# Performance work log

Measured on AMD Instinct MI355X. Metric: run time of the kernel, lower is better.

The kernel has to match this reference:

```python
import jax, jax.numpy as jnp
import numpy as np

E4M3 = jnp.float8_e4m3fn  # forward fp8 dtype (HYBRID recipe fwd)

def fp8_qdq(x, fp8_dtype):
    # quantize (scale=1) to fp8 then dequantize back: models precision loss
    return x.astype(fp8_dtype).astype(x.dtype)

def setup_inputs() -> dict:
    key = jax.random.key(0)
    k1, k2 = jax.random.split(key)
    tokens, d_in, units = 4096, 1024, 4096
    x = jax.random.normal(k1, (tokens, d_in), dtype=jnp.float32)
    # kernel_initializer default: RandomNormal(mean=0.0, stddev=0.023)
    kernel = jax.random.normal(k2, (d_in, units), dtype=jnp.float32) * 0.023
    bias = jnp.zeros((units,), dtype=jnp.float32)
    return {"x": x, "kernel": kernel, "bias": bias}

def reference(x, kernel, bias):
    # fp8 quantize/dequantize prologue on activations and weights
    xq = fp8_qdq(x, E4M3)          # [tokens, d_in]
    kq = fp8_qdq(kernel, E4M3)     # [d_in, units]
    out = jnp.matmul(xq, kq) + bias  # [tokens, units]
    # gelu approximate=True (tanh approximation)
    return jax.nn.gelu(out, approximate=True)
```

## Files before the change

kernel.cpp:

```cpp
#include <hip/hip_runtime.h>
#include <hip/hip_bf16.h>

typedef float f32x4 __attribute__((ext_vector_type(4)));
typedef long  l2    __attribute__((ext_vector_type(2)));

__device__ __forceinline__ void gld16(const void* g, void* l) {
    __builtin_amdgcn_global_load_lds(
        (const __attribute__((address_space(1))) void*)g,
        (__attribute__((address_space(3))) void*)l,
        16, 0, 0);
}

__device__ __forceinline__ float gelu_tanh(float x) {
    float u = 0.7978845608028654f * x * (1.0f + 0.044715f * x * x);
    float e = __expf(2.0f * u);
    float t = 1.0f - 2.0f / (e + 1.0f);
    return 0.5f * x * (1.0f + t);
}


__global__ __launch_bounds__(256) void quant_fused_kernel(
        const float* __restrict__ x,  unsigned char* __restrict__ Aq,
        const float* __restrict__ w,  unsigned char* __restrict__ BTq,
        int nA, int K, int N) {
    __shared__ unsigned char lds[64 * 68];
    const int tid = threadIdx.x;

    if (blockIdx.x < nA) {
        int i = blockIdx.x * 256 + tid;
        float4 v = reinterpret_cast<const float4*>(x)[i];
        int pk = 0;
        pk = __builtin_amdgcn_cvt_pk_fp8_f32(v.x, v.y, pk, false);
        pk = __builtin_amdgcn_cvt_pk_fp8_f32(v.z, v.w, pk, true);
        const long k4 = (long)i * 4;
        const int  row = (int)(k4 / K);
        const int  k   = (int)(k4 % K);
        const int  o   = k & 63;
        const int  g   = (o & 31) >> 3;
        const int  s   = (o & 7) + ((o >> 5) & 1) * 8;
        const int  c   = g ^ ((row >> 1) & 3);
        *reinterpret_cast<unsigned int*>(
            Aq + (long)row * K + (k & ~63) + (c << 4) + s) = (unsigned int)pk;
        return;
    }

    const int bid = blockIdx.x - nA;
    const int n0 = (bid & (N / 64 - 1)) * 64;
    const int k0 = (bid / (N / 64)) * 64;

    #pragma unroll
    for (int p = 0; p < 4; ++p) {
        int s = p * 256 + tid;
        int r = s >> 4;
        int c = s & 15;
        float4 v = *reinterpret_cast<const float4*>(
            w + (long)(k0 + r) * N + n0 + c * 4);
        int pk = 0;
        pk = __builtin_amdgcn_cvt_pk_fp8_f32(v.x, v.y, pk, false);
        pk = __builtin_amdgcn_cvt_pk_fp8_f32(v.z, v.w, pk, true);
        *reinterpret_cast<unsigned int*>(&lds[r * 68 + c * 4]) = (unsigned int)pk;
    }
    __syncthreads();
    #pragma unroll
    for (int p = 0; p < 4; ++p) {
        int sidx = p * 256 + tid;
        int n  = sidx >> 4;
        int kg = sidx & 15;
        unsigned int wv = 0;
        #pragma unroll
        for (int j = 0; j < 4; ++j)
            wv |= (unsigned int)lds[(kg * 4 + j) * 68 + n] << (8 * j);
        const int nn = n0 + n;
        const int o  = kg * 4;
        const int g  = (o & 31) >> 3;
        const int s  = (o & 7) + ((o >> 5) & 1) * 8;
        const int c  = g ^ ((nn >> 1) & 3);
        *reinterpret_cast<unsigned int*>(
            BTq + (long)nn * K + k0 + (c << 4) + s) = wv;
    }
}

__global__ __launch_bounds__(512, 4) void gemm_fp8_kernel(
        const unsigned char* __restrict__ A,
        const unsigned char* __restrict__ BT,
        const float* __restrict__ bias,
        float* __restrict__ out,
        int M, int N, int K) {
    constexpr int BM = 128, BN = 256, BK = 64;
    __shared__ unsigned char lds[2][(BM + BN) * BK];

    const int tid  = threadIdx.x;
    const int lane = tid & 63;
    const int wid  = tid >> 6;
    const int wm   = wid >> 2;
    const int wn   = wid & 3;

    const int bid = blockIdx.x;
    const int xcd = bid & 7, idx = bid >> 3;
    const int tile_m = (xcd >> 1) * 8 + (idx & 7);
    const int tile_n = (xcd & 1) * 8 + (idx >> 3);
    const int m0 = tile_m * BM, n0 = tile_n * BN;

    const int lrow = lane & 15;
    const int kgrp = lane >> 4;
    const int chunkoff = ((kgrp ^ ((lrow >> 1) & 3)) << 4);

    const int srow   = tid >> 2;
    const int schunk = (tid & 3) << 4;
    const unsigned char* gA = A  + (long)(m0 + srow) * K + schunk;
    const unsigned char* gB = BT + (long)(n0 + srow) * K + schunk;

    const int aBase = (wm * 64 + lrow) * 64 + chunkoff;
    const int bBase = 8192 + (wn * 64 + lrow) * 64 + chunkoff;

    f32x4 acc[4][4] = {};

    const int NT = K / BK;

#define STAGE_A(BB, TT)                                                   \
    gld16(gA + (long)(TT) * BK, &lds[BB][wid * 1024])
#define STAGE_B(BB, H, TT)                                                \
    gld16(gB + (long)(H) * 128 * K + (long)(TT) * BK,                     \
          &lds[BB][8192 + (H) * 8192 + wid * 1024])

#define MFMA_Q(AI0, BJ0, AR, BR)                                          \
    _Pragma("unroll") for (int ks = 0; ks < 2; ++ks)                      \
    _Pragma("unroll") for (int fi = 0; fi < 2; ++fi)                      \
    _Pragma("unroll") for (int fj = 0; fj < 2; ++fj)                      \
        acc[(AI0) + fi][(BJ0) + fj] =                                     \
            __builtin_amdgcn_mfma_f32_16x16x32_fp8_fp8(                   \
                AR[fi][ks], BR[fj][ks], acc[(AI0) + fi][(BJ0) + fj], 0, 0, 0)

    STAGE_A(0, 0); STAGE_B(0, 0, 0); STAGE_B(0, 1, 0);
    asm volatile("s_waitcnt vmcnt(0)" ::: "memory");
    __builtin_amdgcn_s_barrier();

    for (int t = 0; t < NT; ++t) {
        const int cur = t & 1, nxt = cur ^ 1;
        const unsigned char* sL = &lds[cur][0];
        const bool st = (t + 1 < NT);
        l2 a01[2], a23[2], b01[2], b23[2];

        if (st) { STAGE_A(nxt, t + 1); STAGE_B(nxt, 0, t + 1); }
        #pragma unroll
        for (int f = 0; f < 2; ++f) {
            a01[f] = *reinterpret_cast<const l2*>(sL + aBase + f * 1024);
            b01[f] = *reinterpret_cast<const l2*>(sL + bBase + f * 1024);
            b23[f] = *reinterpret_cast<const l2*>(sL + bBase + 2048 + f * 1024);
        }
        __builtin_amdgcn_s_barrier();
        asm volatile("s_waitcnt lgkmcnt(0)" ::: "memory");
        __builtin_amdgcn_sched_barrier(0);
        __builtin_amdgcn_s_setprio(1);
        MFMA_Q(0, 0, a01, b01);
        MFMA_Q(0, 2, a01, b23);
        __builtin_amdgcn_s_setprio(0);

        if (st) { STAGE_B(nxt, 1, t + 1); }
        #pragma unroll
        for (int f = 0; f < 2; ++f)
            a23[f] = *reinterpret_cast<const l2*>(sL + aBase + 2048 + f * 1024);
        __builtin_amdgcn_s_barrier();
        asm volatile("s_waitcnt lgkmcnt(0)" ::: "memory");
        __builtin_amdgcn_sched_barrier(0);
        __builtin_amdgcn_s_setprio(1);
        MFMA_Q(2, 0, a23, b01);
        MFMA_Q(2, 2, a23, b23);
        __builtin_amdgcn_s_setprio(0);
        __builtin_amdgcn_sched_barrier(0);

        if (t < NT - 1) {
            asm volatile("s_waitcnt vmcnt(0)" ::: "memory");
            __builtin_amdgcn_sched_barrier(0);
            __builtin_amdgcn_s_barrier();
        }
    }

    __syncthreads();
    float* eplds = reinterpret_cast<float*>(&lds[0][0]) + wid * 1088;
    const int  col0   = n0 + wn * 64;
    const long rbase0 = m0 + wm * 64;
    float bv[4];
    #pragma unroll
    for (int bj = 0; bj < 4; ++bj) bv[bj] = bias[col0 + bj * 16 + lrow];

    #pragma unroll
    for (int ai = 0; ai < 4; ++ai) {
        #pragma unroll
        for (int bj = 0; bj < 4; ++bj) {
            #pragma unroll
            for (int r = 0; r < 4; ++r) {
                float xv = acc[ai][bj][r] + bv[bj];
                eplds[(kgrp * 4 + r) * 68 + bj * 16 + lrow] = gelu_tanh(xv);
            }
        }
        #pragma unroll
        for (int s = 0; s < 4; ++s) {
            f32x4 v = *reinterpret_cast<const f32x4*>(
                eplds + (s * 4 + kgrp) * 68 + lrow * 4);
            __builtin_nontemporal_store(v, reinterpret_cast<f32x4*>(
                out + (rbase0 + ai * 16 + s * 4 + kgrp) * N + col0 + lrow * 4));
        }
    }
#undef STAGE_A
#undef STAGE_B
#undef MFMA_Q
}

extern "C" void kernel_launch(void* const* d_in, const int* in_sizes, int n_in,
                              void* d_out, int out_size, void* d_ws, size_t ws_size,
                              hipStream_t stream) {
    const float* x    = (const float*)d_in[0];
    const float* w    = (const float*)d_in[1];
    const float* bias = (const float*)d_in[2];
    float* out = (float*)d_out;

    const int units  = in_sizes[2];
    const int dmodel = in_sizes[1] / units;
    const int tokens = in_sizes[0] / dmodel;

    unsigned char* Aq  = (unsigned char*)d_ws;
    unsigned char* BTq = Aq + (size_t)tokens * dmodel;

    const int nA = tokens * dmodel / 4 / 256;
    const int nB = (units / 64) * (dmodel / 64);
    quant_fused_kernel<<<dim3(nA + nB), dim3(256), 0, stream>>>(
        x, Aq, w, BTq, nA, dmodel, units);

    const int nblocks = (tokens / 128) * (units / 256);
    gemm_fp8_kernel<<<dim3(nblocks), dim3(512), 0, stream>>>(
        Aq, BTq, bias, out, tokens, units, dmodel);
}
```

Before: 47.36 us.

## Load GEMM operands directly from global into registers, drop LDS staging

Replaces the LDS double-buffered global_load_lds pipeline with direct per-lane global loads of pre-swizzled fp8 fragments into registers, software-pipelined two K-steps deep. The tile shrinks to 128x128 with 256-thread blocks, giving twice as many blocks, and the LDS is used only for the epilogue. This removes LDS traffic and barriers, but it gives up cross-wave reuse of each tile through LDS. Operands are re-fetched from L2 by each wave, and the loads are 16-byte strided reads spread across rows.

```diff
diff --git a/kernel.cpp b/kernel.cpp
--- a/kernel.cpp
+++ b/kernel.cpp
@@ -3,13 +3,6 @@
 
 typedef float f32x4 __attribute__((ext_vector_type(4)));
 typedef long  l2    __attribute__((ext_vector_type(2)));
-
-__device__ __forceinline__ void gld16(const void* g, void* l) {
-    __builtin_amdgcn_global_load_lds(
-        (const __attribute__((address_space(1))) void*)g,
-        (__attribute__((address_space(3))) void*)l,
-        16, 0, 0);
-}
 
 __device__ __forceinline__ float gelu_tanh(float x) {
     float u = 0.7978845608028654f * x * (1.0f + 0.044715f * x * x);
@@ -80,104 +73,65 @@
     }
 }
 
-__global__ __launch_bounds__(512, 4) void gemm_fp8_kernel(
+__global__ __launch_bounds__(256, 3) void gemm_fp8_kernel(
         const unsigned char* __restrict__ A,
         const unsigned char* __restrict__ BT,
         const float* __restrict__ bias,
         float* __restrict__ out,
         int M, int N, int K) {
-    constexpr int BM = 128, BN = 256, BK = 64;
-    __shared__ unsigned char lds[2][(BM + BN) * BK];
+    constexpr int BM = 128, BN = 128, BK = 64;
+    __shared__ float eplds_all[4][1088];
 
     const int tid  = threadIdx.x;
     const int lane = tid & 63;
     const int wid  = tid >> 6;
-    const int wm   = wid >> 2;
-    const int wn   = wid & 3;
+    const int wm   = wid >> 1, wn = wid & 1;
 
     const int bid = blockIdx.x;
     const int xcd = bid & 7, idx = bid >> 3;
-    const int tile_m = (xcd >> 1) * 8 + (idx & 7);
-    const int tile_n = (xcd & 1) * 8 + (idx >> 3);
+    const int tile_m = (xcd >> 1) * 8  + (idx & 7);
+    const int tile_n = (xcd & 1) * 16 + (idx >> 3);
     const int m0 = tile_m * BM, n0 = tile_n * BN;
 
     const int lrow = lane & 15;
     const int kgrp = lane >> 4;
     const int chunkoff = ((kgrp ^ ((lrow >> 1) & 3)) << 4);
 
-    const int srow   = tid >> 2;
-    const int schunk = (tid & 3) << 4;
-    const unsigned char* gA = A  + (long)(m0 + srow) * K + schunk;
-    const unsigned char* gB = BT + (long)(n0 + srow) * K + schunk;
-
-    const int aBase = (wm * 64 + lrow) * 64 + chunkoff;
-    const int bBase = 8192 + (wn * 64 + lrow) * 64 + chunkoff;
+    const unsigned char* pA[4];
+    const unsigned char* pB[4];
+    #pragma unroll
+    for (int f = 0; f < 4; ++f) {
+        pA[f] = A  + (long)(m0 + wm * 64 + f * 16 + lrow) * K + chunkoff;
+        pB[f] = BT + (long)(n0 + wn * 64 + f * 16 + lrow) * K + chunkoff;
+    }
 
     f32x4 acc[4][4] = {};
+    l2 aX[4], bX[4], aY[4], bY[4];
 
     const int NT = K / BK;
 
-#define STAGE_A(BB, TT)                                                   \
-    gld16(gA + (long)(TT) * BK, &lds[BB][wid * 1024])
-#define STAGE_B(BB, H, TT)                                                \
-    gld16(gB + (long)(H) * 128 * K + (long)(TT) * BK,                     \
-          &lds[BB][8192 + (H) * 8192 + wid * 1024])
-
-#define MFMA_Q(AI0, BJ0, AR, BR)                                          \
-    _Pragma("unroll") for (int ks = 0; ks < 2; ++ks)                      \
-    _Pragma("unroll") for (int fi = 0; fi < 2; ++fi)                      \
-    _Pragma("unroll") for (int fj = 0; fj < 2; ++fj)                      \
-        acc[(AI0) + fi][(BJ0) + fj] =                                     \
-            __builtin_amdgcn_mfma_f32_16x16x32_fp8_fp8(                   \
-                AR[fi][ks], BR[fj][ks], acc[(AI0) + fi][(BJ0) + fj], 0, 0, 0)
-
-    STAGE_A(0, 0); STAGE_B(0, 0, 0); STAGE_B(0, 1, 0);
-    asm volatile("s_waitcnt vmcnt(0)" ::: "memory");
-    __builtin_amdgcn_s_barrier();
-
-    for (int t = 0; t < NT; ++t) {
-        const int cur = t & 1, nxt = cur ^ 1;
-        const unsigned char* sL = &lds[cur][0];
-        const bool st = (t + 1 < NT);
-        l2 a01[2], a23[2], b01[2], b23[2];
-
-        if (st) { STAGE_A(nxt, t + 1); STAGE_B(nxt, 0, t + 1); }
-        #pragma unroll
-        for (int f = 0; f < 2; ++f) {
-            a01[f] = *reinterpret_cast<const l2*>(sL + aBase + f * 1024);
-            b01[f] = *reinterpret_cast<const l2*>(sL + bBase + f * 1024);
-            b23[f] = *reinterpret_cast<const l2*>(sL + bBase + 2048 + f * 1024);
-        }
-        __builtin_amdgcn_s_barrier();
-        asm volatile("s_waitcnt lgkmcnt(0)" ::: "memory");
-        __builtin_amdgcn_sched_barrier(0);
-        __builtin_amdgcn_s_setprio(1);
-        MFMA_Q(0, 0, a01, b01);
-        MFMA_Q(0, 2, a01, b23);
-        __builtin_amdgcn_s_setprio(0);
-
-        if (st) { STAGE_B(nxt, 1, t + 1); }
-        #pragma unroll
-        for (int f = 0; f < 2; ++f)
-            a23[f] = *reinterpret_cast<const l2*>(sL + aBase + 2048 + f * 1024);
-        __builtin_amdgcn_s_barrier();
-        asm volatile("s_waitcnt lgkmcnt(0)" ::: "memory");
-        __builtin_amdgcn_sched_barrier(0);
-        __builtin_amdgcn_s_setprio(1);
-        MFMA_Q(2, 0, a23, b01);
-        MFMA_Q(2, 2, a23, b23);
-        __builtin_amdgcn_s_setprio(0);
-        __builtin_amdgcn_sched_barrier(0);
-
-        if (t < NT - 1) {
-            asm volatile("s_waitcnt vmcnt(0)" ::: "memory");
-            __builtin_amdgcn_sched_barrier(0);
-            __builtin_amdgcn_s_barrier();
-        }
+#define LOADS(AS, BS, T)                                                  \
+    _Pragma("unroll") for (int f = 0; f < 4; ++f) {                       \
+        AS[f] = *reinterpret_cast<const l2*>(pA[f] + (T) * 64);           \
+        BS[f] = *reinterpret_cast<const l2*>(pB[f] + (T) * 64);           \
     }
 
-    __syncthreads();
-    float* eplds = reinterpret_cast<float*>(&lds[0][0]) + wid * 1088;
+#define MFMA_ALL(AR, BR)                                                  \
+    _Pragma("unroll") for (int ks = 0; ks < 2; ++ks)                      \
+    _Pragma("unroll") for (int fi = 0; fi < 4; ++fi)                      \
+    _Pragma("unroll") for (int fj = 0; fj < 4; ++fj)                      \
+        acc[fi][fj] = __builtin_amdgcn_mfma_f32_16x16x32_fp8_fp8(         \
+            AR[fi][ks], BR[fj][ks], acc[fi][fj], 0, 0, 0)
+
+    LOADS(aX, bX, 0);
+    for (int t = 0; t < NT; t += 2) {
+        LOADS(aY, bY, t + 1);
+        MFMA_ALL(aX, bX);
+        if (t + 2 < NT) { LOADS(aX, bX, t + 2); }
+        MFMA_ALL(aY, bY);
+    }
+
+    float* eplds = eplds_all[wid];
     const int  col0   = n0 + wn * 64;
     const long rbase0 = m0 + wm * 64;
     float bv[4];
@@ -202,9 +156,8 @@
                 out + (rbase0 + ai * 16 + s * 4 + kgrp) * N + col0 + lrow * 4));
         }
     }
-#undef STAGE_A
-#undef STAGE_B
-#undef MFMA_Q
+#undef LOADS
+#undef MFMA_ALL
 }
 
 extern "C" void kernel_launch(void* const* d_in, const int* in_sizes, int n_in,
@@ -227,7 +180,7 @@
     quant_fused_kernel<<<dim3(nA + nB), dim3(256), 0, stream>>>(
         x, Aq, w, BTq, nA, dmodel, units);
 
-    const int nblocks = (tokens / 128) * (units / 256);
-    gemm_fp8_kernel<<<dim3(nblocks), dim3(512), 0, stream>>>(
+    const int nblocks = (tokens / 128) * (units / 128);
+    gemm_fp8_kernel<<<dim3(nblocks), dim3(256), 0, stream>>>(
         Aq, BTq, bias, out, tokens, units, dmodel);
 }
```

After: 56.87 us. 20.1% more time.

## Shrink GEMM tile to 128x128 with 4x2 wave layout and higher occupancy

Applied to the files above, without the earlier changes.

Halves the GEMM block tile along N (BN 256 to 128) and remaps the 8 waves into a 4x2 grid, each holding a 32x64 accumulator instead of 64x64. The block count doubles and launch bounds are raised to 8 waves per SIMD, aiming for more resident blocks and less register pressure to better hide latency. Shared memory becomes a union so the epilogue scratch fits inside the smaller staging buffer. The cost is lower arithmetic intensity per block, with more global and LDS traffic per MFMA, and fewer MFMAs between barriers.

```diff
diff --git a/kernel.cpp b/kernel.cpp
--- a/kernel.cpp
+++ b/kernel.cpp
@@ -80,25 +80,28 @@
     }
 }
 
-__global__ __launch_bounds__(512, 4) void gemm_fp8_kernel(
+__global__ __launch_bounds__(512, 8) void gemm_fp8_kernel(
         const unsigned char* __restrict__ A,
         const unsigned char* __restrict__ BT,
         const float* __restrict__ bias,
         float* __restrict__ out,
         int M, int N, int K) {
-    constexpr int BM = 128, BN = 256, BK = 64;
-    __shared__ unsigned char lds[2][(BM + BN) * BK];
+    constexpr int BM = 128, BN = 128, BK = 64;
+    __shared__ union {
+        unsigned char buf[2][(BM + BN) * BK];
+        float ep[8][1088];
+    } sm;
 
     const int tid  = threadIdx.x;
     const int lane = tid & 63;
     const int wid  = tid >> 6;
-    const int wm   = wid >> 2;
-    const int wn   = wid & 3;
+    const int wm   = wid >> 1;
+    const int wn   = wid & 1;
 
     const int bid = blockIdx.x;
     const int xcd = bid & 7, idx = bid >> 3;
-    const int tile_m = (xcd >> 1) * 8 + (idx & 7);
-    const int tile_n = (xcd & 1) * 8 + (idx >> 3);
+    const int tile_m = (xcd >> 1) * 8  + (idx & 7);
+    const int tile_n = (xcd & 1) * 16 + (idx >> 3);
     const int m0 = tile_m * BM, n0 = tile_n * BN;
 
     const int lrow = lane & 15;
@@ -110,62 +113,57 @@
     const unsigned char* gA = A  + (long)(m0 + srow) * K + schunk;
     const unsigned char* gB = BT + (long)(n0 + srow) * K + schunk;
 
-    const int aBase = (wm * 64 + lrow) * 64 + chunkoff;
+    const int aBase = (wm * 32 + lrow) * 64 + chunkoff;
     const int bBase = 8192 + (wn * 64 + lrow) * 64 + chunkoff;
 
-    f32x4 acc[4][4] = {};
+    f32x4 acc[2][4] = {};
 
     const int NT = K / BK;
 
 #define STAGE_A(BB, TT)                                                   \
-    gld16(gA + (long)(TT) * BK, &lds[BB][wid * 1024])
-#define STAGE_B(BB, H, TT)                                                \
-    gld16(gB + (long)(H) * 128 * K + (long)(TT) * BK,                     \
-          &lds[BB][8192 + (H) * 8192 + wid * 1024])
-
-#define MFMA_Q(AI0, BJ0, AR, BR)                                          \
+    gld16(gA + (long)(TT) * BK, &sm.buf[BB][wid * 1024])
+#define STAGE_B(BB, TT)                                                   \
+    gld16(gB + (long)(TT) * BK, &sm.buf[BB][8192 + wid * 1024])
+
+#define MFMA_Q(BJ0, BR)                                                   \
     _Pragma("unroll") for (int ks = 0; ks < 2; ++ks)                      \
     _Pragma("unroll") for (int fi = 0; fi < 2; ++fi)                      \
     _Pragma("unroll") for (int fj = 0; fj < 2; ++fj)                      \
-        acc[(AI0) + fi][(BJ0) + fj] =                                     \
-            __builtin_amdgcn_mfma_f32_16x16x32_fp8_fp8(                   \
-                AR[fi][ks], BR[fj][ks], acc[(AI0) + fi][(BJ0) + fj], 0, 0, 0)
-
-    STAGE_A(0, 0); STAGE_B(0, 0, 0); STAGE_B(0, 1, 0);
+        acc[fi][(BJ0) + fj] = __builtin_amdgcn_mfma_f32_16x16x32_fp8_fp8( \
+            a01[fi][ks], BR[fj][ks], acc[fi][(BJ0) + fj], 0, 0, 0)
+
+    STAGE_A(0, 0); STAGE_B(0, 0);
     asm volatile("s_waitcnt vmcnt(0)" ::: "memory");
     __builtin_amdgcn_s_barrier();
 
     for (int t = 0; t < NT; ++t) {
         const int cur = t & 1, nxt = cur ^ 1;
-        const unsigned char* sL = &lds[cur][0];
+        const unsigned char* sL = &sm.buf[cur][0];
         const bool st = (t + 1 < NT);
-        l2 a01[2], a23[2], b01[2], b23[2];
-
-        if (st) { STAGE_A(nxt, t + 1); STAGE_B(nxt, 0, t + 1); }
+        l2 a01[2], b01[2], b23[2];
+
+        if (st) { STAGE_A(nxt, t + 1); }
         #pragma unroll
         for (int f = 0; f < 2; ++f) {
             a01[f] = *reinterpret_cast<const l2*>(sL + aBase + f * 1024);
             b01[f] = *reinterpret_cast<const l2*>(sL + bBase + f * 1024);
-            b23[f] = *reinterpret_cast<const l2*>(sL + bBase + 2048 + f * 1024);
         }
         __builtin_amdgcn_s_barrier();
         asm volatile("s_waitcnt lgkmcnt(0)" ::: "memory");
         __builtin_amdgcn_sched_barrier(0);
         __builtin_amdgcn_s_setprio(1);
-        MFMA_Q(0, 0, a01, b01);
-        MFMA_Q(0, 2, a01, b23);
+        MFMA_Q(0, b01);
         __builtin_amdgcn_s_setprio(0);
 
-        if (st) { STAGE_B(nxt, 1, t + 1); }
+        if (st) { STAGE_B(nxt, t + 1); }
         #pragma unroll
         for (int f = 0; f < 2; ++f)
-            a23[f] = *reinterpret_cast<const l2*>(sL + aBase + 2048 + f * 1024);
+            b23[f] = *reinterpret_cast<const l2*>(sL + bBase + 2048 + f * 1024);
         __builtin_amdgcn_s_barrier();
         asm volatile("s_waitcnt lgkmcnt(0)" ::: "memory");
         __builtin_amdgcn_sched_barrier(0);
         __builtin_amdgcn_s_setprio(1);
-        MFMA_Q(2, 0, a23, b01);
-        MFMA_Q(2, 2, a23, b23);
+        MFMA_Q(2, b23);
         __builtin_amdgcn_s_setprio(0);
         __builtin_amdgcn_sched_barrier(0);
 
@@ -177,15 +175,15 @@
     }
 
     __syncthreads();
-    float* eplds = reinterpret_cast<float*>(&lds[0][0]) + wid * 1088;
+    float* eplds = sm.ep[wid];
     const int  col0   = n0 + wn * 64;
-    const long rbase0 = m0 + wm * 64;
+    const long rbase0 = m0 + wm * 32;
     float bv[4];
     #pragma unroll
     for (int bj = 0; bj < 4; ++bj) bv[bj] = bias[col0 + bj * 16 + lrow];
 
     #pragma unroll
-    for (int ai = 0; ai < 4; ++ai) {
+    for (int ai = 0; ai < 2; ++ai) {
         #pragma unroll
         for (int bj = 0; bj < 4; ++bj) {
             #pragma unroll
@@ -227,7 +225,7 @@
     quant_fused_kernel<<<dim3(nA + nB), dim3(256), 0, stream>>>(
         x, Aq, w, BTq, nA, dmodel, units);
 
-    const int nblocks = (tokens / 128) * (units / 256);
+    const int nblocks = (tokens / 128) * (units / 128);
     gemm_fp8_kernel<<<dim3(nblocks), dim3(512), 0, stream>>>(
         Aq, BTq, bias, out, tokens, units, dmodel);
 }
```

Measured after the change: 48.19 us. Within noise of the previous version (+1.8%).

## Switch GEMM to 32x32x16 fp8 MFMA with matching operand layout

Applied to the files above, without the earlier changes.

The GEMM inner loop moves from 16x16x32 fp8 MFMAs to 32x32x16 fp8 MFMAs, with four 16-wide accumulators per wave instead of sixteen 4-wide ones. The quantize kernel's byte permutation and swizzle are changed so each lane's LDS fragment matches the new instruction's operand layout. The epilogue is rewritten for the 32x32 accumulator layout and uses a padded 33-float LDS stride to transpose before the vector stores. The intent is fewer, larger MFMA issues and simpler fragment bookkeeping. The odd LDS stride makes the 16-byte epilogue reads unaligned, and the extra waitcnts add some serialization.

```diff
diff --git a/kernel.cpp b/kernel.cpp
--- a/kernel.cpp
+++ b/kernel.cpp
@@ -1,8 +1,9 @@
 #include <hip/hip_runtime.h>
 #include <hip/hip_bf16.h>
 
-typedef float f32x4 __attribute__((ext_vector_type(4)));
-typedef long  l2    __attribute__((ext_vector_type(2)));
+typedef float f32x4  __attribute__((ext_vector_type(4)));
+typedef float f32x16 __attribute__((ext_vector_type(16)));
+typedef long  l2     __attribute__((ext_vector_type(2)));
 
 __device__ __forceinline__ void gld16(const void* g, void* l) {
     __builtin_amdgcn_global_load_lds(
@@ -36,11 +37,12 @@
         const int  row = (int)(k4 / K);
         const int  k   = (int)(k4 % K);
         const int  o   = k & 63;
-        const int  g   = (o & 31) >> 3;
-        const int  s   = (o & 7) + ((o >> 5) & 1) * 8;
-        const int  c   = g ^ ((row >> 1) & 3);
+        const int  s   = o >> 4;
+        const int  h   = (o >> 3) & 1;
+        const int  c2  = (((s >> 1) << 1) | h) ^ ((row >> 1) & 3);
         *reinterpret_cast<unsigned int*>(
-            Aq + (long)row * K + (k & ~63) + (c << 4) + s) = (unsigned int)pk;
+            Aq + (long)row * K + (k & ~63) + (c2 << 4) + ((s & 1) << 3) + (k & 7))
+            = (unsigned int)pk;
         return;
     }
 
@@ -70,13 +72,13 @@
         #pragma unroll
         for (int j = 0; j < 4; ++j)
             wv |= (unsigned int)lds[(kg * 4 + j) * 68 + n] << (8 * j);
-        const int nn = n0 + n;
-        const int o  = kg * 4;
-        const int g  = (o & 31) >> 3;
-        const int s  = (o & 7) + ((o >> 5) & 1) * 8;
-        const int c  = g ^ ((nn >> 1) & 3);
+        const int nn  = n0 + n;
+        const int s   = kg >> 2;
+        const int h   = (kg >> 1) & 1;
+        const int c2  = (((s >> 1) << 1) | h) ^ ((nn >> 1) & 3);
         *reinterpret_cast<unsigned int*>(
-            BTq + (long)nn * K + k0 + (c << 4) + s) = wv;
+            BTq + (long)nn * K + k0 + (c2 << 4) + ((s & 1) << 3) + ((kg & 1) * 4))
+            = wv;
     }
 }
 
@@ -87,7 +89,10 @@
         float* __restrict__ out,
         int M, int N, int K) {
     constexpr int BM = 128, BN = 256, BK = 64;
-    __shared__ unsigned char lds[2][(BM + BN) * BK];
+    __shared__ union {
+        unsigned char buf[2][(BM + BN) * BK];
+        float ep[8][1056];
+    } sm;
 
     const int tid  = threadIdx.x;
     const int lane = tid & 63;
@@ -101,35 +106,48 @@
     const int tile_n = (xcd & 1) * 8 + (idx >> 3);
     const int m0 = tile_m * BM, n0 = tile_n * BN;
 
-    const int lrow = lane & 15;
-    const int kgrp = lane >> 4;
-    const int chunkoff = ((kgrp ^ ((lrow >> 1) & 3)) << 4);
+    const int l31 = lane & 31;
+    const int h   = lane >> 5;
 
     const int srow   = tid >> 2;
     const int schunk = (tid & 3) << 4;
     const unsigned char* gA = A  + (long)(m0 + srow) * K + schunk;
     const unsigned char* gB = BT + (long)(n0 + srow) * K + schunk;
 
-    const int aBase = (wm * 64 + lrow) * 64 + chunkoff;
-    const int bBase = 8192 + (wn * 64 + lrow) * 64 + chunkoff;
-
-    f32x4 acc[4][4] = {};
+    int offA[2][2], offB[2][2];
+    #pragma unroll
+    for (int f = 0; f < 2; ++f) {
+        const int rA = wm * 64 + f * 32 + l31;
+        const int rB = wn * 64 + f * 32 + l31;
+        const int xA = (rA >> 1) & 3, xB = (rB >> 1) & 3;
+        #pragma unroll
+        for (int p = 0; p < 2; ++p) {
+            offA[f][p] = rA * 64 + ((((p << 1) | h) ^ xA) << 4);
+            offB[f][p] = 8192 + rB * 64 + ((((p << 1) | h) ^ xB) << 4);
+        }
+    }
+
+    f32x16 acc00 = {}, acc01 = {}, acc10 = {}, acc11 = {};
 
     const int NT = K / BK;
 
 #define STAGE_A(BB, TT)                                                   \
-    gld16(gA + (long)(TT) * BK, &lds[BB][wid * 1024])
+    gld16(gA + (long)(TT) * BK, &sm.buf[BB][wid * 1024])
 #define STAGE_B(BB, H, TT)                                                \
     gld16(gB + (long)(H) * 128 * K + (long)(TT) * BK,                     \
-          &lds[BB][8192 + (H) * 8192 + wid * 1024])
-
-#define MFMA_Q(AI0, BJ0, AR, BR)                                          \
-    _Pragma("unroll") for (int ks = 0; ks < 2; ++ks)                      \
-    _Pragma("unroll") for (int fi = 0; fi < 2; ++fi)                      \
-    _Pragma("unroll") for (int fj = 0; fj < 2; ++fj)                      \
-        acc[(AI0) + fi][(BJ0) + fj] =                                     \
-            __builtin_amdgcn_mfma_f32_16x16x32_fp8_fp8(                   \
-                AR[fi][ks], BR[fj][ks], acc[(AI0) + fi][(BJ0) + fj], 0, 0, 0)
+          &sm.buf[BB][8192 + (H) * 8192 + wid * 1024])
+
+#define MFMA8(P)                                                          \
+    do {                                                                  \
+        acc00 = __builtin_amdgcn_mfma_f32_32x32x16_fp8_fp8(a0[0], b0[0], acc00, 0, 0, 0); \
+        acc01 = __builtin_amdgcn_mfma_f32_32x32x16_fp8_fp8(a0[0], b1[0], acc01, 0, 0, 0); \
+        acc10 = __builtin_amdgcn_mfma_f32_32x32x16_fp8_fp8(a1[0], b0[0], acc10, 0, 0, 0); \
+        acc11 = __builtin_amdgcn_mfma_f32_32x32x16_fp8_fp8(a1[0], b1[0], acc11, 0, 0, 0); \
+        acc00 = __builtin_amdgcn_mfma_f32_32x32x16_fp8_fp8(a0[1], b0[1], acc00, 0, 0, 0); \
+        acc01 = __builtin_amdgcn_mfma_f32_32x32x16_fp8_fp8(a0[1], b1[1], acc01, 0, 0, 0); \
+        acc10 = __builtin_amdgcn_mfma_f32_32x32x16_fp8_fp8(a1[1], b0[1], acc10, 0, 0, 0); \
+        acc11 = __builtin_amdgcn_mfma_f32_32x32x16_fp8_fp8(a1[1], b1[1], acc11, 0, 0, 0); \
+    } while (0)
 
     STAGE_A(0, 0); STAGE_B(0, 0, 0); STAGE_B(0, 1, 0);
     asm volatile("s_waitcnt vmcnt(0)" ::: "memory");
@@ -137,35 +155,32 @@
 
     for (int t = 0; t < NT; ++t) {
         const int cur = t & 1, nxt = cur ^ 1;
-        const unsigned char* sL = &lds[cur][0];
+        const unsigned char* sL = &sm.buf[cur][0];
         const bool st = (t + 1 < NT);
-        l2 a01[2], a23[2], b01[2], b23[2];
+        l2 a0, a1, b0, b1;
 
         if (st) { STAGE_A(nxt, t + 1); STAGE_B(nxt, 0, t + 1); }
-        #pragma unroll
-        for (int f = 0; f < 2; ++f) {
-            a01[f] = *reinterpret_cast<const l2*>(sL + aBase + f * 1024);
-            b01[f] = *reinterpret_cast<const l2*>(sL + bBase + f * 1024);
-            b23[f] = *reinterpret_cast<const l2*>(sL + bBase + 2048 + f * 1024);
-        }
+        a0 = *reinterpret_cast<const l2*>(sL + offA[0][0]);
+        a1 = *reinterpret_cast<const l2*>(sL + offA[1][0]);
+        b0 = *reinterpret_cast<const l2*>(sL + offB[0][0]);
+        b1 = *reinterpret_cast<const l2*>(sL + offB[1][0]);
         __builtin_amdgcn_s_barrier();
         asm volatile("s_waitcnt lgkmcnt(0)" ::: "memory");
         __builtin_amdgcn_sched_barrier(0);
         __builtin_amdgcn_s_setprio(1);
-        MFMA_Q(0, 0, a01, b01);
-        MFMA_Q(0, 2, a01, b23);
+        MFMA8(0);
         __builtin_amdgcn_s_setprio(0);
 
         if (st) { STAGE_B(nxt, 1, t + 1); }
-        #pragma unroll
-        for (int f = 0; f < 2; ++f)
-            a23[f] = *reinterpret_cast<const l2*>(sL + aBase + 2048 + f * 1024);
+        a0 = *reinterpret_cast<const l2*>(sL + offA[0][1]);
+        a1 = *reinterpret_cast<const l2*>(sL + offA[1][1]);
+        b0 = *reinterpret_cast<const l2*>(sL + offB[0][1]);
+        b1 = *reinterpret_cast<const l2*>(sL + offB[1][1]);
         __builtin_amdgcn_s_barrier();
         asm volatile("s_waitcnt lgkmcnt(0)" ::: "memory");
         __builtin_amdgcn_sched_barrier(0);
         __builtin_amdgcn_s_setprio(1);
-        MFMA_Q(2, 0, a23, b01);
-        MFMA_Q(2, 2, a23, b23);
+        MFMA8(1);
         __builtin_amdgcn_s_setprio(0);
         __builtin_amdgcn_sched_barrier(0);
 
@@ -177,34 +192,40 @@
     }
 
     __syncthreads();
-    float* eplds = reinterpret_cast<float*>(&lds[0][0]) + wid * 1088;
+    float* eplds = sm.ep[wid];
     const int  col0   = n0 + wn * 64;
     const long rbase0 = m0 + wm * 64;
-    float bv[4];
-    #pragma unroll
-    for (int bj = 0; bj < 4; ++bj) bv[bj] = bias[col0 + bj * 16 + lrow];
-
-    #pragma unroll
-    for (int ai = 0; ai < 4; ++ai) {
-        #pragma unroll
-        for (int bj = 0; bj < 4; ++bj) {
-            #pragma unroll
-            for (int r = 0; r < 4; ++r) {
-                float xv = acc[ai][bj][r] + bv[bj];
-                eplds[(kgrp * 4 + r) * 68 + bj * 16 + lrow] = gelu_tanh(xv);
-            }
-        }
-        #pragma unroll
-        for (int s = 0; s < 4; ++s) {
-            f32x4 v = *reinterpret_cast<const f32x4*>(
-                eplds + (s * 4 + kgrp) * 68 + lrow * 4);
-            __builtin_nontemporal_store(v, reinterpret_cast<f32x4*>(
-                out + (rbase0 + ai * 16 + s * 4 + kgrp) * N + col0 + lrow * 4));
-        }
-    }
+    const float bv0 = bias[col0 + l31];
+    const float bv1 = bias[col0 + 32 + l31];
+
+#define EPI(ACC, FI, FJ, BV)                                              \
+    do {                                                                  \
+        _Pragma("unroll")                                                 \
+        for (int r = 0; r < 16; ++r) {                                    \
+            const int row = (r & 3) + 8 * (r >> 2) + 4 * h;               \
+            eplds[row * 33 + l31] = gelu_tanh(ACC[r] + (BV));             \
+        }                                                                 \
+        asm volatile("s_waitcnt lgkmcnt(0)" ::: "memory");                \
+        _Pragma("unroll")                                                 \
+        for (int ps = 0; ps < 4; ++ps) {                                  \
+            const int rr = ps * 8 + (lane >> 3);                          \
+            f32x4 v = *reinterpret_cast<const f32x4*>(                    \
+                eplds + rr * 33 + (lane & 7) * 4);                        \
+            __builtin_nontemporal_store(v, reinterpret_cast<f32x4*>(      \
+                out + (rbase0 + (FI) * 32 + rr) * N + col0 + (FJ) * 32    \
+                    + (lane & 7) * 4));                                   \
+        }                                                                 \
+        asm volatile("s_waitcnt lgkmcnt(0)" ::: "memory");                \
+    } while (0)
+
+    EPI(acc00, 0, 0, bv0);
+    EPI(acc01, 0, 1, bv1);
+    EPI(acc10, 1, 0, bv0);
+    EPI(acc11, 1, 1, bv1);
 #undef STAGE_A
 #undef STAGE_B
-#undef MFMA_Q
+#undef MFMA8
+#undef EPI
 }
 
 extern "C" void kernel_launch(void* const* d_in, const int* in_sizes, int n_in,
```

After: 52.02 us. 9.8% more time.
